# Kernel tuning notes

Measured on AMD Instinct MI355X. Metric: run time of the kernel, lower is better.

## Reference

```python
import jax, jax.numpy as jnp
import numpy as np

B = 65536          # batch (number of states)
M = 32             # obstacles per state -> x width = 2*M
PHI = [4, 64, 64, 64]
RHO = [64, 64, 64, 32]


def _init_mlp(key, dims, prefix):
    params = {}
    ks = jax.random.split(key, len(dims) - 1)
    for i, (din, dout) in enumerate(zip(dims[:-1], dims[1:])):
        scale = 1.0 / np.sqrt(din)
        params[f"{prefix}_W{i+1}"] = scale * jax.random.normal(ks[i], (din, dout), dtype=jnp.float32)
        params[f"{prefix}_b{i+1}"] = jnp.zeros((dout,), dtype=jnp.float32)
    return params


def setup_inputs() -> dict:
    key = jax.random.key(0)
    kx, kv, kphi, krho = jax.random.split(key, 4)
    inp = {
        "x": jax.random.normal(kx, (B, 2 * M), dtype=jnp.float32),
        "vel": jax.random.normal(kv, (B, 2), dtype=jnp.float32),
    }
    inp.update(_init_mlp(kphi, PHI, "phi"))
    inp.update(_init_mlp(krho, RHO, "rho"))
    return inp


def _mlp3(h, W1, b1, W2, b2, W3, b3):
    # FeedForward: activation between hidden layers, linear output
    h = jax.nn.relu(h @ W1 + b1)
    h = jax.nn.relu(h @ W2 + b2)
    return h @ W3 + b3


def reference(x, vel,
              phi_W1, phi_b1, phi_W2, phi_b2, phi_W3, phi_b3,
              rho_W1, rho_b1, rho_W2, rho_b2, rho_W3, rho_b3):
    b = x.shape[0]
    m = x.shape[1] // 2
    obs = x.reshape(b, m, 2)                                   # [B, M, 2]
    velb = jnp.broadcast_to(vel[:, None, :], (b, m, 2))        # [B, M, 2]
    inp = jnp.concatenate([obs, velb], axis=-1)                # [B, M, 4]
    # phi batched across all obstacle elements (replaces the per-i loop)
    h = _mlp3(inp, phi_W1, phi_b1, phi_W2, phi_b2, phi_W3, phi_b3)  # [B, M, 64]
    X = h.sum(axis=1)                                          # DeepSets sum pool -> [B, 64]
    return _mlp3(X, rho_W1, rho_b1, rho_W2, rho_b2, rho_W3, rho_b3)  # [B, 32]
```

## Files before the change

kernel.cpp:

```cpp
#include <hip/hip_runtime.h>

typedef _Float16 h16x8 __attribute__((ext_vector_type(8)));
typedef _Float16 h16x4 __attribute__((ext_vector_type(4)));
typedef _Float16 h16x2 __attribute__((ext_vector_type(2)));
typedef float    fx4   __attribute__((ext_vector_type(4)));

static __device__ __forceinline__ fx4 mfma16(h16x8 a, h16x8 b, fx4 c) {
  return __builtin_amdgcn_mfma_f32_16x16x32_f16(a, b, c, 0, 0, 0);
}
static __device__ __forceinline__ h16x2 pkrtz(float a, float b) {
  auto r = __builtin_amdgcn_cvt_pkrtz(a, b);
  h16x2 o; __builtin_memcpy(&o, &r, sizeof(o)); return o;
}
union ABfrag { h16x2 p[4]; h16x8 v; };
union H4     { h16x2 p[2]; h16x4 v; };


__global__ __launch_bounds__(512, 4)
void deepset_main(const float* __restrict__ x,   const float* __restrict__ vel,
                  const float* __restrict__ pW1, const float* __restrict__ pb1,
                  const float* __restrict__ pW2, const float* __restrict__ pb2,
                  const float* __restrict__ pW3, const float* __restrict__ pb3,
                  const float* __restrict__ rW1, const float* __restrict__ rb1,
                  const float* __restrict__ rW2, const float* __restrict__ rb2,
                  const float* __restrict__ rW3, const float* __restrict__ rb3,
                  float* __restrict__ out)
{
  __shared__ __align__(16) _Float16 L2T[64][72];
  __shared__ __align__(16) _Float16 L3T[64][72];
  __shared__ __align__(16) _Float16 Q1T[64][72];
  __shared__ __align__(16) _Float16 Q2T[64][72];
  __shared__ __align__(16) _Float16 Q3T[32][72];
  __shared__ __align__(16) _Float16 xh[8][16][72];

  const int tid  = threadIdx.x;
  const int wave = tid >> 6;
  const int lane = tid & 63;
  const int q    = lane >> 4;
  const int c    = lane & 15;
  const int sBase = blockIdx.x * 128;
  const int sWave = sBase + wave * 16;

  {
    const int p  = tid >> 3;
    const int cg = (tid & 7) * 8;
    const int f  = 16*(p & 3) + (p >> 2);
    const fx4 w2a = *(const fx4*)(pW2 + p*64 + cg);
    const fx4 w2b = *(const fx4*)(pW2 + p*64 + cg + 4);
    const fx4 w3a = *(const fx4*)(pW3 + f*64 + cg);
    const fx4 w3b = *(const fx4*)(pW3 + f*64 + cg + 4);
    const fx4 r1a = *(const fx4*)(rW1 + f*64 + cg);
    const fx4 r1b = *(const fx4*)(rW1 + f*64 + cg + 4);
    const fx4 r2a = *(const fx4*)(rW2 + f*64 + cg);
    const fx4 r2b = *(const fx4*)(rW2 + f*64 + cg + 4);
#pragma unroll
    for (int i = 0; i < 4; ++i) {
      L2T[cg + i][p]     = (_Float16)w2a[i];
      L2T[cg + 4 + i][p] = (_Float16)w2b[i];
      L3T[cg + i][p]     = (_Float16)w3a[i];
      L3T[cg + 4 + i][p] = (_Float16)w3b[i];
      Q1T[cg + i][p]     = (_Float16)r1a[i];
      Q1T[cg + 4 + i][p] = (_Float16)r1b[i];
      Q2T[cg + i][p]     = (_Float16)r2a[i];
      Q2T[cg + 4 + i][p] = (_Float16)r2b[i];
    }
    if (tid < 256) {
      const int p3  = tid >> 2;
      const int cg3 = (tid & 3) * 8;
      const int f3  = 16*(p3 & 3) + (p3 >> 2);
      const fx4 r3a = *(const fx4*)(rW3 + f3*32 + cg3);
      const fx4 r3b = *(const fx4*)(rW3 + f3*32 + cg3 + 4);
#pragma unroll
      for (int i = 0; i < 4; ++i) {
        Q3T[cg3 + i][p3]     = (_Float16)r3a[i];
        Q3T[cg3 + 4 + i][p3] = (_Float16)r3b[i];
      }
    }
  }

  {
    const int s0 = lane >> 2, ch = (lane & 3) * 16;
#pragma unroll
    for (int k = 0; k < 4; ++k) {
      const fx4 g = *(const fx4*)(x + (size_t)(sWave + s0)*64 + ch + 4*k);
      H4 pk; pk.p[0] = pkrtz(g[0], g[1]); pk.p[1] = pkrtz(g[2], g[3]);
      *(h16x4*)&xh[wave][s0][ch + 4*k] = pk.v;
    }
  }
  const float2 vc = *(const float2*)(vel + 2*(size_t)(sWave + c));

  h16x2 wx[2][4], wy[2][4], vbp[2][4];
#pragma unroll
  for (int ks = 0; ks < 2; ++ks)
#pragma unroll
    for (int t = 0; t < 4; ++t) {
      const int f0 = 32*ks + 8*q + 2*t;
      wx[ks][t] = pkrtz(pW1[f0], pW1[f0 + 1]);
      wy[ks][t] = pkrtz(pW1[64 + f0], pW1[64 + f0 + 1]);
      const float v0 = fmaf(vc.x, pW1[128 + f0],     fmaf(vc.y, pW1[192 + f0],     pb1[f0]));
      const float v1 = fmaf(vc.x, pW1[128 + f0 + 1], fmaf(vc.y, pW1[192 + f0 + 1], pb1[f0 + 1]));
      vbp[ks][t] = pkrtz(v0, v1);
    }
  float b2v[4];
#pragma unroll
  for (int ct = 0; ct < 4; ++ct) b2v[ct] = pb2[16*ct + c];

  __syncthreads();

  h16x8 B2[4][2];
#pragma unroll
  for (int ct = 0; ct < 4; ++ct)
#pragma unroll
    for (int ks = 0; ks < 2; ++ks)
      B2[ct][ks] = *(const h16x8*)&L2T[16*ct + c][32*ks + 8*q];

  const h16x2 z2 = {(_Float16)0.f, (_Float16)0.f};
  const fx4 zf4 = {0.f, 0.f, 0.f, 0.f};
  fx4 Xacc[4] = {zf4, zf4, zf4, zf4};

  h16x4 p_cur = *(const h16x4*)&xh[wave][c][0];
#pragma unroll 1
  for (int oo = 0; oo < 16; ++oo) {
    h16x4 p_nxt;
    if (oo < 15) p_nxt = *(const h16x4*)&xh[wave][c][4*(oo + 1)];
#pragma unroll
    for (int hh = 0; hh < 2; ++hh) {
      h16x2 ox, oy;
      ox[0] = p_cur[2*hh];     ox[1] = p_cur[2*hh];
      oy[0] = p_cur[2*hh + 1]; oy[1] = p_cur[2*hh + 1];
      h16x8 A1[2];
#pragma unroll
      for (int ks = 0; ks < 2; ++ks) {
        ABfrag a;
#pragma unroll
        for (int t = 0; t < 4; ++t) {
          const h16x2 h = ox * wx[ks][t] + oy * wy[ks][t] + vbp[ks][t];
          a.p[t] = __builtin_elementwise_max(h, z2);
        }
        A1[ks] = a.v;
      }
#pragma unroll
      for (int ct = 0; ct < 4; ++ct) {
        fx4 acc = {b2v[ct], b2v[ct], b2v[ct], b2v[ct]};
        acc = mfma16(A1[0], B2[ct][0], acc);
        acc = mfma16(A1[1], B2[ct][1], acc);
        Xacc[ct] += __builtin_elementwise_max(acc, zf4);
      }
    }
    p_cur = p_nxt;
  }

  _Float16 (*h2T)[72] = xh[wave];

#pragma unroll
  for (int r = 0; r < 4; ++r) {
    H4 pk;
    pk.p[0] = pkrtz(Xacc[0][r], Xacc[1][r]);
    pk.p[1] = pkrtz(Xacc[2][r], Xacc[3][r]);
    *(h16x4*)&h2T[4*q + r][4*c] = pk.v;
  }
  h16x8 B3[4][2];
#pragma unroll
  for (int ct = 0; ct < 4; ++ct)
#pragma unroll
    for (int ks = 0; ks < 2; ++ks)
      B3[ct][ks] = *(const h16x8*)&L3T[16*ct + c][32*ks + 8*q];
  float b3s[4];
#pragma unroll
  for (int ct = 0; ct < 4; ++ct) b3s[ct] = 32.f * pb3[16*ct + c];

  __builtin_amdgcn_s_waitcnt(0xC07F);
  __builtin_amdgcn_wave_barrier();
  h16x8 AX[2];
#pragma unroll
  for (int ks = 0; ks < 2; ++ks)
    AX[ks] = *(const h16x8*)&h2T[c][32*ks + 8*q];
  __builtin_amdgcn_wave_barrier();

  fx4 C3[4];
#pragma unroll
  for (int ct = 0; ct < 4; ++ct) {
    fx4 acc = {b3s[ct], b3s[ct], b3s[ct], b3s[ct]};
    acc = mfma16(AX[0], B3[ct][0], acc);
    acc = mfma16(AX[1], B3[ct][1], acc);
    C3[ct] = acc;
  }
#pragma unroll
  for (int r = 0; r < 4; ++r) {
    H4 pk;
    pk.p[0] = pkrtz(C3[0][r], C3[1][r]);
    pk.p[1] = pkrtz(C3[2][r], C3[3][r]);
    *(h16x4*)&h2T[4*q + r][4*c] = pk.v;
  }
  h16x8 R1[4][2];
#pragma unroll
  for (int ct = 0; ct < 4; ++ct)
#pragma unroll
    for (int ks = 0; ks < 2; ++ks)
      R1[ct][ks] = *(const h16x8*)&Q1T[16*ct + c][32*ks + 8*q];
  float rb1v[4];
#pragma unroll
  for (int ct = 0; ct < 4; ++ct) rb1v[ct] = rb1[16*ct + c];

  __builtin_amdgcn_s_waitcnt(0xC07F);
  __builtin_amdgcn_wave_barrier();
  h16x8 A1r[2];
#pragma unroll
  for (int ks = 0; ks < 2; ++ks)
    A1r[ks] = *(const h16x8*)&h2T[c][32*ks + 8*q];
  __builtin_amdgcn_wave_barrier();

  fx4 D1[4];
#pragma unroll
  for (int ct = 0; ct < 4; ++ct) {
    fx4 acc = {rb1v[ct], rb1v[ct], rb1v[ct], rb1v[ct]};
    acc = mfma16(A1r[0], R1[ct][0], acc);
    acc = mfma16(A1r[1], R1[ct][1], acc);
    D1[ct] = __builtin_elementwise_max(acc, zf4);
  }
#pragma unroll
  for (int r = 0; r < 4; ++r) {
    H4 pk;
    pk.p[0] = pkrtz(D1[0][r], D1[1][r]);
    pk.p[1] = pkrtz(D1[2][r], D1[3][r]);
    *(h16x4*)&h2T[4*q + r][4*c] = pk.v;
  }
  h16x8 R2[4][2];
#pragma unroll
  for (int ct = 0; ct < 4; ++ct)
#pragma unroll
    for (int ks = 0; ks < 2; ++ks)
      R2[ct][ks] = *(const h16x8*)&Q2T[16*ct + c][32*ks + 8*q];
  float rb2v[4];
#pragma unroll
  for (int ct = 0; ct < 4; ++ct) rb2v[ct] = rb2[16*ct + c];

  __builtin_amdgcn_s_waitcnt(0xC07F);
  __builtin_amdgcn_wave_barrier();
  h16x8 A2r[2];
#pragma unroll
  for (int ks = 0; ks < 2; ++ks)
    A2r[ks] = *(const h16x8*)&h2T[c][32*ks + 8*q];
  __builtin_amdgcn_wave_barrier();

  fx4 D2[4];
#pragma unroll
  for (int ct = 0; ct < 4; ++ct) {
    fx4 acc = {rb2v[ct], rb2v[ct], rb2v[ct], rb2v[ct]};
    acc = mfma16(A2r[0], R2[ct][0], acc);
    acc = mfma16(A2r[1], R2[ct][1], acc);
    D2[ct] = __builtin_elementwise_max(acc, zf4);
  }
#pragma unroll
  for (int r = 0; r < 4; ++r) {
    H4 pk;
    pk.p[0] = pkrtz(D2[0][r], D2[1][r]);
    pk.p[1] = pkrtz(D2[2][r], D2[3][r]);
    *(h16x4*)&h2T[4*q + r][4*c] = pk.v;
  }
  h16x8 R3[2][2];
#pragma unroll
  for (int ct = 0; ct < 2; ++ct)
#pragma unroll
    for (int ks = 0; ks < 2; ++ks)
      R3[ct][ks] = *(const h16x8*)&Q3T[16*ct + c][32*ks + 8*q];
  float rb3v[2];
#pragma unroll
  for (int ct = 0; ct < 2; ++ct) rb3v[ct] = rb3[16*ct + c];

  __builtin_amdgcn_s_waitcnt(0xC07F);
  __builtin_amdgcn_wave_barrier();
  h16x8 A3r[2];
#pragma unroll
  for (int ks = 0; ks < 2; ++ks)
    A3r[ks] = *(const h16x8*)&h2T[c][32*ks + 8*q];
  __builtin_amdgcn_wave_barrier();

  fx4 D3[2];
#pragma unroll
  for (int ct = 0; ct < 2; ++ct) {
    fx4 acc = {rb3v[ct], rb3v[ct], rb3v[ct], rb3v[ct]};
    acc = mfma16(A3r[0], R3[ct][0], acc);
    acc = mfma16(A3r[1], R3[ct][1], acc);
    D3[ct] = acc;
  }
  const int srow = sWave + 4*q;
#pragma unroll
  for (int ct = 0; ct < 2; ++ct)
#pragma unroll
    for (int r = 0; r < 4; ++r)
      out[(size_t)(srow + r)*32 + 16*ct + c] = D3[ct][r];
}

extern "C" void kernel_launch(void* const* d_in, const int* in_sizes, int n_in,
                              void* d_out, int out_size, void* d_ws, size_t ws_size,
                              hipStream_t stream) {
  const float* x   = (const float*)d_in[0];
  const float* vel = (const float*)d_in[1];
  const float* pW1 = (const float*)d_in[2];
  const float* pb1 = (const float*)d_in[3];
  const float* pW2 = (const float*)d_in[4];
  const float* pb2 = (const float*)d_in[5];
  const float* pW3 = (const float*)d_in[6];
  const float* pb3 = (const float*)d_in[7];
  const float* rW1 = (const float*)d_in[8];
  const float* rb1 = (const float*)d_in[9];
  const float* rW2 = (const float*)d_in[10];
  const float* rb2 = (const float*)d_in[11];
  const float* rW3 = (const float*)d_in[12];
  const float* rb3 = (const float*)d_in[13];
  float* out = (float*)d_out;

  const int B = in_sizes[0] / 64;
  deepset_main<<<dim3(B / 128), dim3(512), 0, stream>>>(
      x, vel, pW1, pb1, pW2, pb2, pW3, pb3,
      rW1, rb1, rW2, rb2, rW3, rb3, out);
}
```

Before: 121.7 us.

## Accumulate phi sum-pool in packed fp16 and vectorize weight transpose staging

The phi layer-2 outputs are converted to packed fp16 right after each MFMA, and the ReLU plus sum-pool accumulation runs as packed half2 ops instead of fp32 vector adds. This roughly halves the VALU work and accumulator registers in the hot loop. The price is summing 32 obstacles in fp16, which loses precision and could overflow. The weight staging now does coalesced scalar loads and 16-byte LDS stores instead of scattered 2-byte transposed stores, and the prefetch branch in the loop is made unconditional with a wrapped index.

Result: faster. 113.8 us (-6.5%).

```diff
diff --git a/kernel.cpp b/kernel.cpp
--- a/kernel.cpp
+++ b/kernel.cpp
@@ -42,39 +42,40 @@
   const int sWave = sBase + wave * 16;
 
   {
-    const int p  = tid >> 3;
-    const int cg = (tid & 7) * 8;
-    const int f  = 16*(p & 3) + (p >> 2);
-    const fx4 w2a = *(const fx4*)(pW2 + p*64 + cg);
-    const fx4 w2b = *(const fx4*)(pW2 + p*64 + cg + 4);
-    const fx4 w3a = *(const fx4*)(pW3 + f*64 + cg);
-    const fx4 w3b = *(const fx4*)(pW3 + f*64 + cg + 4);
-    const fx4 r1a = *(const fx4*)(rW1 + f*64 + cg);
-    const fx4 r1b = *(const fx4*)(rW1 + f*64 + cg + 4);
-    const fx4 r2a = *(const fx4*)(rW2 + f*64 + cg);
-    const fx4 r2b = *(const fx4*)(rW2 + f*64 + cg + 4);
-#pragma unroll
-    for (int i = 0; i < 4; ++i) {
-      L2T[cg + i][p]     = (_Float16)w2a[i];
-      L2T[cg + 4 + i][p] = (_Float16)w2b[i];
-      L3T[cg + i][p]     = (_Float16)w3a[i];
-      L3T[cg + 4 + i][p] = (_Float16)w3b[i];
-      Q1T[cg + i][p]     = (_Float16)r1a[i];
-      Q1T[cg + 4 + i][p] = (_Float16)r1b[i];
-      Q2T[cg + i][p]     = (_Float16)r2a[i];
-      Q2T[cg + 4 + i][p] = (_Float16)r2b[i];
-    }
+    const int col = tid & 63;
+    const int kg  = tid >> 6;
+    float v2[8], v3[8], r1[8], r2[8];
+#pragma unroll
+    for (int j = 0; j < 8; ++j) {
+      const int p = 8*kg + j;
+      const int f = 16*(p & 3) + (p >> 2);
+      v2[j] = pW2[p*64 + col];
+      v3[j] = pW3[f*64 + col];
+      r1[j] = rW1[f*64 + col];
+      r2[j] = rW2[f*64 + col];
+    }
+    h16x8 h2v, h3v, h1v, h2r;
+#pragma unroll
+    for (int j = 0; j < 8; ++j) { h2v[j] = (_Float16)v2[j]; h3v[j] = (_Float16)v3[j];
+                                  h1v[j] = (_Float16)r1[j]; h2r[j] = (_Float16)r2[j]; }
+    *(h16x8*)&L2T[col][8*kg] = h2v;
+    *(h16x8*)&L3T[col][8*kg] = h3v;
+    *(h16x8*)&Q1T[col][8*kg] = h1v;
+    *(h16x8*)&Q2T[col][8*kg] = h2r;
     if (tid < 256) {
-      const int p3  = tid >> 2;
-      const int cg3 = (tid & 3) * 8;
-      const int f3  = 16*(p3 & 3) + (p3 >> 2);
-      const fx4 r3a = *(const fx4*)(rW3 + f3*32 + cg3);
-      const fx4 r3b = *(const fx4*)(rW3 + f3*32 + cg3 + 4);
-#pragma unroll
-      for (int i = 0; i < 4; ++i) {
-        Q3T[cg3 + i][p3]     = (_Float16)r3a[i];
-        Q3T[cg3 + 4 + i][p3] = (_Float16)r3b[i];
+      const int col3 = tid & 31;
+      const int kg3  = tid >> 5;
+      float r3[8];
+#pragma unroll
+      for (int j = 0; j < 8; ++j) {
+        const int p = 8*kg3 + j;
+        const int f = 16*(p & 3) + (p >> 2);
+        r3[j] = rW3[f*32 + col3];
       }
+      h16x8 h3r;
+#pragma unroll
+      for (int j = 0; j < 8; ++j) h3r[j] = (_Float16)r3[j];
+      *(h16x8*)&Q3T[col3][8*kg3] = h3r;
     }
   }
 
@@ -115,14 +116,12 @@
       B2[ct][ks] = *(const h16x8*)&L2T[16*ct + c][32*ks + 8*q];
 
   const h16x2 z2 = {(_Float16)0.f, (_Float16)0.f};
-  const fx4 zf4 = {0.f, 0.f, 0.f, 0.f};
-  fx4 Xacc[4] = {zf4, zf4, zf4, zf4};
+  h16x2 Xh[4][2] = {{z2, z2}, {z2, z2}, {z2, z2}, {z2, z2}};
 
   h16x4 p_cur = *(const h16x4*)&xh[wave][c][0];
 #pragma unroll 1
   for (int oo = 0; oo < 16; ++oo) {
-    h16x4 p_nxt;
-    if (oo < 15) p_nxt = *(const h16x4*)&xh[wave][c][4*(oo + 1)];
+    h16x4 p_nxt = *(const h16x4*)&xh[wave][c][4*((oo + 1) & 15)];
 #pragma unroll
     for (int hh = 0; hh < 2; ++hh) {
       h16x2 ox, oy;
@@ -144,7 +143,10 @@
         fx4 acc = {b2v[ct], b2v[ct], b2v[ct], b2v[ct]};
         acc = mfma16(A1[0], B2[ct][0], acc);
         acc = mfma16(A1[1], B2[ct][1], acc);
-        Xacc[ct] += __builtin_elementwise_max(acc, zf4);
+        const h16x2 lo = pkrtz(acc[0], acc[1]);
+        const h16x2 hi = pkrtz(acc[2], acc[3]);
+        Xh[ct][0] += __builtin_elementwise_max(lo, z2);
+        Xh[ct][1] += __builtin_elementwise_max(hi, z2);
       }
     }
     p_cur = p_nxt;
@@ -154,10 +156,10 @@
 
 #pragma unroll
   for (int r = 0; r < 4; ++r) {
-    H4 pk;
-    pk.p[0] = pkrtz(Xacc[0][r], Xacc[1][r]);
-    pk.p[1] = pkrtz(Xacc[2][r], Xacc[3][r]);
-    *(h16x4*)&h2T[4*q + r][4*c] = pk.v;
+    h16x4 pk;
+#pragma unroll
+    for (int ct = 0; ct < 4; ++ct) pk[ct] = Xh[ct][r >> 1][r & 1];
+    *(h16x4*)&h2T[4*q + r][4*c] = pk;
   }
   h16x8 B3[4][2];
 #pragma unroll
@@ -210,6 +212,7 @@
     A1r[ks] = *(const h16x8*)&h2T[c][32*ks + 8*q];
   __builtin_amdgcn_wave_barrier();
 
+  const fx4 zf4 = {0.f, 0.f, 0.f, 0.f};
   fx4 D1[4];
 #pragma unroll
   for (int ct = 0; ct < 4; ++ct) {
```
